# Optimization experiments

Measured on AMD Instinct MI355X. Metric: run time of the kernel, lower is better.

The kernel has to match this reference:

```python
import jax, jax.numpy as jnp
import numpy as np

T, B, F = 160, 640, 40          # time-major input [T, B, F]
H, PJ, L = 768, 256, 3          # nb_hidden, nb_proj, nb_layers
FORGET_BIAS = 1.0               # TF LSTMCell default


def _glorot(k, shape):
    std = (2.0 / (shape[0] + shape[1])) ** 0.5
    return jax.random.normal(k, shape, jnp.float32) * std


def setup_inputs() -> dict:
    key = jax.random.key(0)
    ks = jax.random.split(key, 7)
    x = jax.random.normal(ks[0], (T, B, F), jnp.float32)
    # layer 0: input dim F + proj state PJ; layers 1,2: input dim PJ + PJ
    W0 = _glorot(ks[1], (F + PJ, 4 * H)); b0 = jnp.zeros((4 * H,), jnp.float32)
    P0 = _glorot(ks[2], (H, PJ))
    W1 = _glorot(ks[3], (PJ + PJ, 4 * H)); b1 = jnp.zeros((4 * H,), jnp.float32)
    P1 = _glorot(ks[4], (H, PJ))
    W2 = _glorot(ks[5], (PJ + PJ, 4 * H)); b2 = jnp.zeros((4 * H,), jnp.float32)
    P2 = _glorot(ks[6], (H, PJ))
    return {"x": x, "W0": W0, "b0": b0, "P0": P0,
            "W1": W1, "b1": b1, "P1": P1,
            "W2": W2, "b2": b2, "P2": P2}


def _cell(xt, c, h, W, b, P):
    # TF LSTMCell with num_proj: gates on [x, m_prev]; gate order i, j, f, o.
    z = jnp.concatenate([xt, h], axis=-1) @ W + b            # [B, 4H]
    i, j, f, o = jnp.split(z, 4, axis=-1)
    c_new = jax.nn.sigmoid(f + FORGET_BIAS) * c + jax.nn.sigmoid(i) * jnp.tanh(j)
    m = jax.nn.sigmoid(o) * jnp.tanh(c_new)                  # [B, H]
    h_new = m @ P                                            # projected state [B, PJ]
    return c_new, h_new


def reference(x, W0, b0, P0, W1, b1, P1, W2, b2, P2):
    params = ((W0, b0, P0), (W1, b1, P1), (W2, b2, P2))
    Bd = x.shape[1]
    init = tuple((jnp.zeros((Bd, H), x.dtype), jnp.zeros((Bd, PJ), x.dtype))
                 for _ in range(L))

    def step(carry, xt):
        inp = xt
        new = []
        for (c, h), (W, b, P) in zip(carry, params):
            c, h = _cell(inp, c, h, W, b, P)
            new.append((c, h))
            inp = h
        return tuple(new), None

    carry, _ = jax.lax.scan(step, init, x)
    emb = carry[-1][1]                                       # last layer h at final step, [B, PJ]
    # tf.nn.l2_normalize
    return emb / jnp.sqrt(jnp.maximum(jnp.sum(emb * emb, axis=-1, keepdims=True), 1e-12))
```

## Files before the change

kernel.cpp:

```cpp
#include <hip/hip_runtime.h>

#define Bdim 640
#define Hdim 768
#define PJdim 256
#define Tdim 160
#define NSTEP (Tdim + 2)
#define ZS 258

typedef _Float16 half8 __attribute__((ext_vector_type(8)));
typedef float floatx4 __attribute__((ext_vector_type(4)));

constexpr size_t HB_HALFS = 3ull * Bdim * PJdim;
constexpr size_t ZP_OFF   = HB_HALFS * 2;
constexpr size_t MB_OFF   = ZP_OFF + 256;
constexpr size_t MB_HALFS = 3ull * Bdim * Hdim;
constexpr size_t X_OFF    = MB_OFF + MB_HALFS * 2;
constexpr size_t X_HALFS  = (size_t)Tdim * Bdim * 40;
constexpr size_t W_OFF    = X_OFF + X_HALFS * 2;
constexpr size_t W_HALFS  = 36ull * 131072;
constexpr size_t P_OFF    = W_OFF + W_HALFS * 2;
constexpr size_t P_HALFS  = 3ull * 196608;
constexpr size_t C_OFF    = P_OFF + P_HALFS * 2;
constexpr size_t C_BYTES  = 3ull * Bdim * Hdim * 4;

__device__ __forceinline__ float sigm(float v) { return 1.0f / (1.0f + __expf(-v)); }
__device__ __forceinline__ float tanh_fast(float v) { return 2.0f / (1.0f + __expf(-2.0f * v)) - 1.0f; }

__device__ __forceinline__ uint4 ld_coh16(const void* p) {
    const unsigned long long* q = (const unsigned long long*)p;
    unsigned long long a = __hip_atomic_load(q,     __ATOMIC_RELAXED, __HIP_MEMORY_SCOPE_AGENT);
    unsigned long long b = __hip_atomic_load(q + 1, __ATOMIC_RELAXED, __HIP_MEMORY_SCOPE_AGENT);
    uint4 r; r.x = (unsigned)a; r.y = (unsigned)(a >> 32);
    r.z = (unsigned)b; r.w = (unsigned)(b >> 32);
    return r;
}
__device__ __forceinline__ void st_coh16b(void* p, _Float16 h) {
    union { _Float16 h; unsigned short u; } cv; cv.h = h;
    __hip_atomic_store((unsigned short*)p, cv.u, __ATOMIC_RELAXED, __HIP_MEMORY_SCOPE_AGENT);
}

__device__ __forceinline__ void wait1(unsigned* c, unsigned tgt)
{
    if (threadIdx.x == 0) {
        while (__hip_atomic_load(c, __ATOMIC_RELAXED, __HIP_MEMORY_SCOPE_AGENT) < tgt)
            __builtin_amdgcn_s_sleep(1);
    }
    asm volatile("buffer_inv sc0" ::: "memory");
    __syncthreads();
}

__device__ __forceinline__ void pipe_wait(unsigned* c0, unsigned t0, unsigned* c1, unsigned t1)
{
    if (threadIdx.x == 0) {
        if (t0)
            while (__hip_atomic_load(c0, __ATOMIC_RELAXED, __HIP_MEMORY_SCOPE_AGENT) < t0)
                __builtin_amdgcn_s_sleep(1);
        if (c1 && t1)
            while (__hip_atomic_load(c1, __ATOMIC_RELAXED, __HIP_MEMORY_SCOPE_AGENT) < t1)
                __builtin_amdgcn_s_sleep(1);
    }
    asm volatile("buffer_inv sc0" ::: "memory");
    __syncthreads();
}

__device__ __forceinline__ void pipe_sig(unsigned* c)
{
    __syncthreads();
    if (threadIdx.x == 0)
        __hip_atomic_fetch_add(c, 1u, __ATOMIC_RELAXED, __HIP_MEMORY_SCOPE_AGENT);
}

__global__ void repack_kernel(const float* __restrict__ x,
                              const float* __restrict__ W0, const float* __restrict__ W1,
                              const float* __restrict__ W2, const float* __restrict__ P0,
                              const float* __restrict__ P1, const float* __restrict__ P2,
                              _Float16* __restrict__ Wfrag, _Float16* __restrict__ Pfrag,
                              _Float16* __restrict__ x16)
{
    size_t idx = (size_t)blockIdx.x * 256 + threadIdx.x;
    if (idx < W_HALFS) {
        int slab = (int)(idx >> 17);
        int l = slab / 12, ht = slab % 12;
        int r  = (int)(idx & 131071);
        int kc = r >> 13;
        int r2 = r & 8191;
        int g  = r2 >> 11;
        int cf = (r2 >> 9) & 3;
        int u  = r2 & 511;
        int lane = u >> 3, e = u & 7;
        int qd = lane >> 4, ln = lane & 15;
        int k   = kc * 32 + qd * 8 + e;
        int col = g * Hdim + ht * 64 + cf * 16 + ln;
        float v;
        if (l == 0)      v = (k < 296) ? W0[(size_t)k * 3072 + col] : 0.0f;
        else if (l == 1) v = W1[(size_t)k * 3072 + col];
        else             v = W2[(size_t)k * 3072 + col];
        Wfrag[idx] = (_Float16)v;
    } else if (idx < W_HALFS + P_HALFS) {
        size_t i = idx - W_HALFS;
        int l = (int)(i / 196608);
        int r = (int)(i % 196608);
        int cq = r / 49152;
        int r2 = r % 49152;
        int kc = r2 / 2048;
        int r3 = r2 & 2047;
        int cgr = r3 >> 9;
        int u  = r3 & 511;
        int lane = u >> 3, e = u & 7;
        int qd = lane >> 4, ln = lane & 15;
        int k  = kc * 32 + qd * 8 + e;
        int pj = cq * 64 + cgr * 16 + ln;
        const float* P = (l == 0) ? P0 : (l == 1) ? P1 : P2;
        Pfrag[i] = (_Float16)P[(size_t)k * PJdim + pj];
    } else if (idx < W_HALFS + P_HALFS + X_HALFS) {
        size_t i = idx - W_HALFS - P_HALFS;
        x16[i] = (_Float16)x[i];
    }
}

__device__ __forceinline__ void gate_step(
    int l, int b0r, int h0, int t, bool xl,
    const half8 (&Breg)[16][2], float (&c)[16],
    const _Float16* __restrict__ x16, const _Float16* __restrict__ h16,
    const _Float16* __restrict__ zerop, _Float16* __restrict__ mbuf,
    _Float16* __restrict__ Ast, float* __restrict__ zst, const float* __restrict__ bst,
    unsigned* pd, unsigned pdt, unsigned* pdlo, unsigned pdlot, int tid)
{
    const int wv = tid >> 6, lane = tid & 63, qd = lane >> 4, ln = lane & 15;
    const int g = wv >> 1, hh = wv & 1;
    const int qd8 = qd * 8;
    const int rowg = b0r + wv * 16 + ln;

    const _Float16* xt  = x16 + ((size_t)t * Bdim + rowg) * 40;
    const _Float16* h0b = h16 + (size_t)rowg * PJdim - 40;
    const _Float16* lob = (l > 0) ? h16 + ((size_t)(l - 1) * Bdim + rowg) * PJdim : nullptr;
    const _Float16* hib = h16 + ((size_t)l * Bdim + rowg) * PJdim - 256;

    auto srcp = [&](int kc) -> const _Float16* {
        int k = kc * 32 + qd8;
        if (l == 0) return (k < 40) ? xt + k : (k < 296) ? h0b + k : zerop;
        return (k < 256) ? lob + k : hib + k;
    };

    floatx4 acc[8][2];
    const floatx4 fz = {0.f, 0.f, 0.f, 0.f};
#pragma unroll
    for (int i = 0; i < 8; ++i) { acc[i][0] = fz; acc[i][1] = fz; }

    _Float16* Aw = Ast + wv * 512 + lane * 8;

    auto stage_gemm = [&](int kc0, int nkc, bool coh) {
        const int ncp = nkc >> 1;
        uint4 p0 = coh ? ld_coh16(srcp(kc0))     : *(const uint4*)srcp(kc0);
        uint4 p1 = coh ? ld_coh16(srcp(kc0 + 1)) : *(const uint4*)srcp(kc0 + 1);
#pragma unroll
        for (int cp = 0; cp < 5; ++cp) {
            if (cp < ncp) {
                const int s0 = (cp & 1) * 2;
                *(uint4*)(Aw + (size_t)s0 * 4096)       = p0;
                *(uint4*)(Aw + (size_t)(s0 + 1) * 4096) = p1;
                if (cp + 1 < ncp) {
                    p0 = coh ? ld_coh16(srcp(kc0 + 2 * cp + 2)) : *(const uint4*)srcp(kc0 + 2 * cp + 2);
                    p1 = coh ? ld_coh16(srcp(kc0 + 2 * cp + 3)) : *(const uint4*)srcp(kc0 + 2 * cp + 3);
                }
                __syncthreads();
#pragma unroll
                for (int j = 0; j < 2; ++j) {
                    const _Float16* Ab = Ast + (size_t)(s0 + j) * 4096;
                    const int kc = kc0 + 2 * cp + j;
#pragma unroll
                    for (int rf = 0; rf < 8; ++rf) {
                        half8 af = *(const half8*)(Ab + rf * 512 + lane * 8);
                        acc[rf][0] = __builtin_amdgcn_mfma_f32_16x16x32_f16(af, Breg[kc][0], acc[rf][0], 0, 0, 0);
                        acc[rf][1] = __builtin_amdgcn_mfma_f32_16x16x32_f16(af, Breg[kc][1], acc[rf][1], 0, 0, 0);
                    }
                }
            }
        }
    };

    if (pd) wait1(pd, pdt);
    if (l == 0) {
        stage_gemm(0, 10, false);
    } else {
        stage_gemm(8, 8, false);
        if (pdlo) wait1(pdlo, pdlot);
        stage_gemm(0, 8, xl);
    }
    __syncthreads();

#pragma unroll
    for (int rf = 0; rf < 8; ++rf)
#pragma unroll
        for (int cf = 0; cf < 2; ++cf)
#pragma unroll
            for (int r = 0; r < 4; ++r)
                zst[(size_t)(rf * 16 + qd * 4 + r) * ZS + g * 64 + hh * 32 + cf * 16 + ln]
                    = acc[rf][cf][r];
    __syncthreads();

    const int row = tid >> 2, c0 = (tid & 3) * 16;
    const float* zrow = zst + (size_t)row * ZS;
    union { _Float16 h[16]; uint4 v[2]; } pk;
#pragma unroll
    for (int q = 0; q < 4; ++q) {
        const int o = q * 4;
        float4 zi = *(const float4*)(zrow + c0 + o);
        float4 zj = *(const float4*)(zrow + 64 + c0 + o);
        float4 zf = *(const float4*)(zrow + 128 + c0 + o);
        float4 zo = *(const float4*)(zrow + 192 + c0 + o);
        float4 bi = *(const float4*)(bst + c0 + o);
        float4 bj = *(const float4*)(bst + 64 + c0 + o);
        float4 bf = *(const float4*)(bst + 128 + c0 + o);
        float4 bo = *(const float4*)(bst + 192 + c0 + o);
        float cn0 = sigm(zf.x + bf.x) * c[o + 0] + sigm(zi.x + bi.x) * tanh_fast(zj.x + bj.x);
        float cn1 = sigm(zf.y + bf.y) * c[o + 1] + sigm(zi.y + bi.y) * tanh_fast(zj.y + bj.y);
        float cn2 = sigm(zf.z + bf.z) * c[o + 2] + sigm(zi.z + bi.z) * tanh_fast(zj.z + bj.z);
        float cn3 = sigm(zf.w + bf.w) * c[o + 3] + sigm(zi.w + bi.w) * tanh_fast(zj.w + bj.w);
        c[o + 0] = cn0; c[o + 1] = cn1; c[o + 2] = cn2; c[o + 3] = cn3;
        pk.h[o + 0] = (_Float16)(sigm(zo.x + bo.x) * tanh_fast(cn0));
        pk.h[o + 1] = (_Float16)(sigm(zo.y + bo.y) * tanh_fast(cn1));
        pk.h[o + 2] = (_Float16)(sigm(zo.z + bo.z) * tanh_fast(cn2));
        pk.h[o + 3] = (_Float16)(sigm(zo.w + bo.w) * tanh_fast(cn3));
    }
    _Float16* mb = mbuf + ((size_t)l * Bdim + b0r + row) * Hdim + h0 + c0;
    *(uint4*)mb       = pk.v[0];
    *(uint4*)(mb + 8) = pk.v[1];
}

__device__ __forceinline__ void proj_step(
    int l, int b0r, int cq, const half8 (&Preg)[24],
    const _Float16* __restrict__ mbuf, _Float16* __restrict__ h16,
    _Float16* __restrict__ AstA, _Float16* __restrict__ AstB, int tid, bool xstore)
{
    const int wv = tid >> 6, lane = tid & 63, qd = lane >> 4, ln = lane & 15;
    const int rh = wv >> 2, cgi = wv & 3;
    const int rowg = b0r + wv * 16 + ln;
    const _Float16* mrow = mbuf + ((size_t)l * Bdim + rowg) * Hdim + qd * 8;
    _Float16* wA = AstA + wv * 512 + lane * 8;
    _Float16* wB = AstB + wv * 512 + lane * 8;

    floatx4 pacc[4];
    const floatx4 fz = {0.f, 0.f, 0.f, 0.f};
#pragma unroll
    for (int i = 0; i < 4; ++i) pacc[i] = fz;

    uint4 p0 = *(const uint4*)(mrow);
    uint4 p1 = *(const uint4*)(mrow + 32);
    uint4 p2 = *(const uint4*)(mrow + 64);
    uint4 p3 = *(const uint4*)(mrow + 96);
#pragma unroll
    for (int ch = 0; ch < 6; ++ch) {
        _Float16* W = (ch & 1) ? wB : wA;
        const _Float16* R = (ch & 1) ? AstB : AstA;
        *(uint4*)(W)                      = p0;
        *(uint4*)(W + (size_t)1 * 4096)   = p1;
        *(uint4*)(W + (size_t)2 * 4096)   = p2;
        *(uint4*)(W + (size_t)3 * 4096)   = p3;
        if (ch < 5) {
            p0 = *(const uint4*)(mrow + (4 * ch + 4) * 32);
            p1 = *(const uint4*)(mrow + (4 * ch + 5) * 32);
            p2 = *(const uint4*)(mrow + (4 * ch + 6) * 32);
            p3 = *(const uint4*)(mrow + (4 * ch + 7) * 32);
        }
        __syncthreads();
#pragma unroll
        for (int kk = 0; kk < 4; ++kk) {
            const _Float16* Ab = R + (size_t)kk * 4096;
#pragma unroll
            for (int rfl = 0; rfl < 4; ++rfl) {
                half8 af = *(const half8*)(Ab + (rh * 4 + rfl) * 512 + lane * 8);
                pacc[rfl] = __builtin_amdgcn_mfma_f32_16x16x32_f16(af, Preg[ch * 4 + kk], pacc[rfl], 0, 0, 0);
            }
        }
    }

    if (xstore) {
#pragma unroll
        for (int rfl = 0; rfl < 4; ++rfl)
#pragma unroll
            for (int r = 0; r < 4; ++r) {
                int row = b0r + (rh * 4 + rfl) * 16 + qd * 4 + r;
                st_coh16b(h16 + ((size_t)l * Bdim + row) * PJdim + cq * 64 + cgi * 16 + ln,
                          (_Float16)pacc[rfl][r]);
            }
    } else {
#pragma unroll
        for (int rfl = 0; rfl < 4; ++rfl)
#pragma unroll
            for (int r = 0; r < 4; ++r) {
                int row = b0r + (rh * 4 + rfl) * 16 + qd * 4 + r;
                h16[((size_t)l * Bdim + row) * PJdim + cq * 64 + cgi * 16 + ln] = (_Float16)pacc[rfl][r];
            }
    }
}

__device__ __forceinline__ void load_Breg(const _Float16* __restrict__ Wfrag, int l, int ht,
                                          int wv, int lane, half8 (&Breg)[16][2])
{
    const int g = wv >> 1, hh = wv & 1;
    const _Float16* wslab = Wfrag + ((size_t)(l * 12 + ht)) * 131072;
#pragma unroll
    for (int kc = 0; kc < 16; ++kc)
#pragma unroll
        for (int cf = 0; cf < 2; ++cf)
            Breg[kc][cf] = *(const half8*)(wslab + kc * 8192 + g * 2048 + (hh * 2 + cf) * 512 + lane * 8);
}

__device__ __forceinline__ void load_Preg(const _Float16* __restrict__ Pfrag, int l, int cq,
                                          int wv, int lane, half8 (&Preg)[24])
{
    const int cgi = wv & 3;
    const _Float16* pslab = Pfrag + (size_t)l * 196608 + (size_t)cq * 49152;
#pragma unroll
    for (int kc = 0; kc < 24; ++kc)
        Preg[kc] = *(const half8*)(pslab + kc * 2048 + cgi * 512 + lane * 8);
}

__device__ __forceinline__ void load_bst(const float* __restrict__ bias, int h0, int tid,
                                         float* __restrict__ bst)
{
    if (tid < 256) {
        int gg = tid >> 6, u = tid & 63;
        bst[tid] = bias[gg * Hdim + h0 + u] + ((gg == 2) ? 1.0f : 0.0f);
    }
}

__device__ __forceinline__ void finalize_row(const _Float16* __restrict__ h16,
                                             float* __restrict__ out, int row, int lane)
{
    const _Float16* e = h16 + ((size_t)2 * Bdim + row) * PJdim + lane * 4;
    float v0 = (float)e[0], v1 = (float)e[1], v2 = (float)e[2], v3 = (float)e[3];
    float ss = v0 * v0 + v1 * v1 + v2 * v2 + v3 * v3;
#pragma unroll
    for (int o = 32; o > 0; o >>= 1) ss += __shfl_xor(ss, o, 64);
    float rs = rsqrtf(fmaxf(ss, 1e-12f));
    float4 o4; o4.x = v0 * rs; o4.y = v1 * rs; o4.z = v2 * rs; o4.w = v3 * rs;
    *(float4*)(out + (size_t)row * PJdim + lane * 4) = o4;
}

__global__ __launch_bounds__(512)
void lstm_persist(const _Float16* __restrict__ x16, const _Float16* __restrict__ Wfrag,
                  const _Float16* __restrict__ Pfrag,
                  const float* __restrict__ bias0, const float* __restrict__ bias1,
                  const float* __restrict__ bias2,
                  _Float16* __restrict__ h16, _Float16* __restrict__ mbuf,
                  const _Float16* __restrict__ zerop, float* __restrict__ out,
                  unsigned* __restrict__ flags)
{
    __shared__ __align__(16) char LDSRAW[133120];
    _Float16* Ast  = (_Float16*)LDSRAW;
    float*    zst  = (float*)LDSRAW;
    float*    bst  = (float*)(LDSRAW + 132096);

    const int tid = threadIdx.x, bid = blockIdx.x;
    const int wv = tid >> 6, lane = tid & 63;

    const int xcd = bid & 7, slot = bid >> 3;
    const int gid = xcd * 2 + (slot >> 4);
    const int rr  = slot & 15;
    if (gid >= 15) return;
    const int bt2 = gid / 3, l = gid % 3;
    const int b0r = bt2 * 128;

    unsigned* gd = flags + (size_t)gid * 64;
    unsigned* pd = gd + 32;

    if (rr < 12) {
        const int ht = rr, h0 = ht * 64;
        const bool xl = ((gid & 1) == 0) && (l > 0);
        half8 Breg[16][2];
        load_Breg(Wfrag, l, ht, wv, lane, Breg);
        load_bst((l == 0) ? bias0 : (l == 1) ? bias1 : bias2, h0, tid, bst);
        float c[16];
#pragma unroll
        for (int u = 0; u < 16; ++u) c[u] = 0.f;
        unsigned* pd_lo = (l > 0) ? flags + (size_t)(gid - 1) * 64 + 32 : nullptr;
        for (int t = 0; t < Tdim; ++t) {
            gate_step(l, b0r, h0, t, xl, Breg, c, x16, h16, zerop, mbuf,
                      Ast, zst, bst,
                      pd, 4u * (unsigned)t,
                      pd_lo, (l > 0) ? 4u * (unsigned)(t + 1) : 0u, tid);
            pipe_sig(gd);
        }
        if (l == 2 && rr < 8) {
            wait1(pd, 4u * (unsigned)Tdim);
            int row0 = b0r + rr * 16 + wv * 2;
            finalize_row(h16, out, row0, lane);
            finalize_row(h16, out, row0 + 1, lane);
        }
    } else {
        const int cq = rr - 12;
        const bool xstore = ((gid & 1) == 1) && (gid + 1 < 15) && ((gid + 1) % 3 != 0);
        half8 Preg[24];
        load_Preg(Pfrag, l, cq, wv, lane, Preg);
        unsigned* gd_hi = (l < 2) ? flags + (size_t)(gid + 1) * 64 : nullptr;
        for (int t = 0; t < Tdim; ++t) {
            pipe_wait(gd, 12u * (unsigned)(t + 1), gd_hi, (l < 2) ? 12u * (unsigned)t : 0u);
            proj_step(l, b0r, cq, Preg, mbuf, h16,
                      Ast, (_Float16*)(LDSRAW + 32768), tid, xstore);
            pipe_sig(pd);
        }
    }
}

__global__ __launch_bounds__(512)
void gate_fb(const _Float16* __restrict__ x16, const _Float16* __restrict__ Wfrag,
             const float* __restrict__ bias0, const float* __restrict__ bias1,
             const float* __restrict__ bias2,
             _Float16* __restrict__ h16, _Float16* __restrict__ mbuf,
             const _Float16* __restrict__ zerop, float* __restrict__ cfb, int s)
{
    __shared__ __align__(16) char LDSRAW[133120];
    _Float16* Ast  = (_Float16*)LDSRAW;
    float*    zst  = (float*)LDSRAW;
    float*    bst  = (float*)(LDSRAW + 132096);
    const int tid = threadIdx.x, bid = blockIdx.x;
    const int ht = bid % 12, z = bid / 12, l = z % 3, bt2 = z / 3;
    const int t = s - l;
    if (t < 0 || t >= Tdim) return;
    const int wv = tid >> 6, lane = tid & 63;
    const int b0r = bt2 * 128, h0 = ht * 64;
    half8 Breg[16][2];
    load_Breg(Wfrag, l, ht, wv, lane, Breg);
    load_bst((l == 0) ? bias0 : (l == 1) ? bias1 : bias2, h0, tid, bst);
    __syncthreads();
    const int row = tid >> 2, c0 = (tid & 3) * 16;
    float c[16];
#pragma unroll
    for (int u = 0; u < 16; ++u)
        c[u] = cfb[((size_t)l * Bdim + b0r + row) * Hdim + h0 + c0 + u];
    gate_step(l, b0r, h0, t, false, Breg, c, x16, h16, zerop, mbuf, Ast, zst, bst,
              nullptr, 0u, nullptr, 0u, tid);
#pragma unroll
    for (int u = 0; u < 16; ++u)
        cfb[((size_t)l * Bdim + b0r + row) * Hdim + h0 + c0 + u] = c[u];
}

__global__ __launch_bounds__(512)
void proj_fb(const _Float16* __restrict__ Pfrag, const _Float16* __restrict__ mbuf,
             _Float16* __restrict__ h16, int s)
{
    __shared__ __align__(16) char LDSRAW[65536];
    const int tid = threadIdx.x, bid = blockIdx.x;
    const int cq = bid & 3, z = bid >> 2, l = z % 3, bt2 = z / 3;
    const int tp = s - l;
    if (tp < 0 || tp >= Tdim) return;
    const int wv = tid >> 6, lane = tid & 63;
    half8 Preg[24];
    load_Preg(Pfrag, l, cq, wv, lane, Preg);
    proj_step(l, bt2 * 128, cq, Preg, mbuf, h16,
              (_Float16*)LDSRAW, (_Float16*)(LDSRAW + 32768), tid, false);
}

__global__ __launch_bounds__(512)
void fin_fb(const _Float16* __restrict__ h16, float* __restrict__ out)
{
    int row = blockIdx.x * 8 + (threadIdx.x >> 6);
    finalize_row(h16, out, row, threadIdx.x & 63);
}

extern "C" void kernel_launch(void* const* d_in, const int* in_sizes, int n_in,
                              void* d_out, int out_size, void* d_ws, size_t ws_size,
                              hipStream_t stream)
{
    (void)in_sizes; (void)n_in; (void)out_size; (void)ws_size;
    const float* x  = (const float*)d_in[0];
    const float* W0 = (const float*)d_in[1];
    const float* b0 = (const float*)d_in[2];
    const float* P0 = (const float*)d_in[3];
    const float* W1 = (const float*)d_in[4];
    const float* b1 = (const float*)d_in[5];
    const float* P1 = (const float*)d_in[6];
    const float* W2 = (const float*)d_in[7];
    const float* b2 = (const float*)d_in[8];
    const float* P2 = (const float*)d_in[9];

    char* ws = (char*)d_ws;
    _Float16* h16   = (_Float16*)(ws);
    _Float16* zerop = (_Float16*)(ws + ZP_OFF);
    _Float16* mbuf  = (_Float16*)(ws + MB_OFF);
    _Float16* x16   = (_Float16*)(ws + X_OFF);
    _Float16* Wfrag = (_Float16*)(ws + W_OFF);
    _Float16* Pfrag = (_Float16*)(ws + P_OFF);
    float*    cfb   = (float*)(ws + C_OFF);
    unsigned* flags = (unsigned*)(ws + C_OFF);
    float*    outp  = (float*)d_out;

    hipMemsetAsync(ws, 0, ZP_OFF + 256, stream);
    hipMemsetAsync(cfb, 0, C_BYTES, stream);

    {
        constexpr size_t total = W_HALFS + P_HALFS + X_HALFS;
        int grid = (int)((total + 255) / 256);
        repack_kernel<<<grid, 256, 0, stream>>>(x, W0, W1, W2, P0, P1, P2, Wfrag, Pfrag, x16);
    }

    int occ = 0;
    hipError_t oe = hipOccupancyMaxActiveBlocksPerMultiprocessor(&occ, lstm_persist, 512, 0);
    bool coop = (oe == hipSuccess && occ >= 1);
    if (coop) {
        void* args[] = { (void*)&x16, (void*)&Wfrag, (void*)&Pfrag,
                         (void*)&b0, (void*)&b1, (void*)&b2,
                         (void*)&h16, (void*)&mbuf, (void*)&zerop, (void*)&outp,
                         (void*)&flags };
        hipError_t le = hipLaunchCooperativeKernel((const void*)lstm_persist,
                                                   dim3(256), dim3(512), args, 0, stream);
        if (le != hipSuccess) { (void)hipGetLastError(); coop = false; }
    }
    if (!coop) {
        for (int s = 0; s < NSTEP; ++s) {
            gate_fb<<<180, 512, 0, stream>>>(x16, Wfrag, b0, b1, b2, h16, mbuf, zerop, cfb, s);
            proj_fb<<<60, 512, 0, stream>>>(Pfrag, mbuf, h16, s);
        }
        fin_fb<<<80, 512, 0, stream>>>(h16, outp);
    }
}
```

Measured before the change: 5.138 ms.

## Use per-hidden-tile flags so projection streams chunks as gate blocks finish

```diff
diff --git a/kernel.cpp b/kernel.cpp
--- a/kernel.cpp
+++ b/kernel.cpp
@@ -49,15 +49,13 @@
     __syncthreads();
 }
 
-__device__ __forceinline__ void pipe_wait(unsigned* c0, unsigned t0, unsigned* c1, unsigned t1)
+__device__ __forceinline__ void wait2(unsigned* a, unsigned* b, unsigned tgt)
 {
     if (threadIdx.x == 0) {
-        if (t0)
-            while (__hip_atomic_load(c0, __ATOMIC_RELAXED, __HIP_MEMORY_SCOPE_AGENT) < t0)
-                __builtin_amdgcn_s_sleep(1);
-        if (c1 && t1)
-            while (__hip_atomic_load(c1, __ATOMIC_RELAXED, __HIP_MEMORY_SCOPE_AGENT) < t1)
-                __builtin_amdgcn_s_sleep(1);
+        while (__hip_atomic_load(a, __ATOMIC_RELAXED, __HIP_MEMORY_SCOPE_AGENT) < tgt)
+            __builtin_amdgcn_s_sleep(1);
+        while (__hip_atomic_load(b, __ATOMIC_RELAXED, __HIP_MEMORY_SCOPE_AGENT) < tgt)
+            __builtin_amdgcn_s_sleep(1);
     }
     asm volatile("buffer_inv sc0" ::: "memory");
     __syncthreads();
@@ -68,6 +66,15 @@
     __syncthreads();
     if (threadIdx.x == 0)
         __hip_atomic_fetch_add(c, 1u, __ATOMIC_RELAXED, __HIP_MEMORY_SCOPE_AGENT);
+}
+
+__device__ __forceinline__ void pipe_sig2(unsigned* a, unsigned* b)
+{
+    __syncthreads();
+    if (threadIdx.x == 0) {
+        __hip_atomic_fetch_add(a, 1u, __ATOMIC_RELAXED, __HIP_MEMORY_SCOPE_AGENT);
+        __hip_atomic_fetch_add(b, 1u, __ATOMIC_RELAXED, __HIP_MEMORY_SCOPE_AGENT);
+    }
 }
 
 __global__ void repack_kernel(const float* __restrict__ x,
@@ -231,7 +238,8 @@
 __device__ __forceinline__ void proj_step(
     int l, int b0r, int cq, const half8 (&Preg)[24],
     const _Float16* __restrict__ mbuf, _Float16* __restrict__ h16,
-    _Float16* __restrict__ AstA, _Float16* __restrict__ AstB, int tid, bool xstore)
+    _Float16* __restrict__ AstA, _Float16* __restrict__ AstB, int tid, bool xstore,
+    unsigned* gdhb, unsigned tgt)
 {
     const int wv = tid >> 6, lane = tid & 63, qd = lane >> 4, ln = lane & 15;
     const int rh = wv >> 2, cgi = wv & 3;
@@ -245,6 +253,7 @@
 #pragma unroll
     for (int i = 0; i < 4; ++i) pacc[i] = fz;
 
+    if (gdhb) wait2(gdhb + 0, gdhb + 16, tgt);
     uint4 p0 = *(const uint4*)(mrow);
     uint4 p1 = *(const uint4*)(mrow + 32);
     uint4 p2 = *(const uint4*)(mrow + 64);
@@ -258,6 +267,8 @@
         *(uint4*)(W + (size_t)2 * 4096)   = p2;
         *(uint4*)(W + (size_t)3 * 4096)   = p3;
         if (ch < 5) {
+            if (gdhb) wait2(gdhb + (size_t)(2 * ch + 2) * 16,
+                            gdhb + (size_t)(2 * ch + 3) * 16, tgt);
             p0 = *(const uint4*)(mrow + (4 * ch + 4) * 32);
             p1 = *(const uint4*)(mrow + (4 * ch + 5) * 32);
             p2 = *(const uint4*)(mrow + (4 * ch + 6) * 32);
@@ -363,25 +374,27 @@
     const int bt2 = gid / 3, l = gid % 3;
     const int b0r = bt2 * 128;
 
-    unsigned* gd = flags + (size_t)gid * 64;
-    unsigned* pd = gd + 32;
+    unsigned* gbase = flags + (size_t)gid * 256;
+    unsigned* gd = gbase;
+    unsigned* pd = gbase + 8;
 
     if (rr < 12) {
         const int ht = rr, h0 = ht * 64;
         const bool xl = ((gid & 1) == 0) && (l > 0);
+        unsigned* gdh_self = gbase + 16 + (size_t)ht * 16;
         half8 Breg[16][2];
         load_Breg(Wfrag, l, ht, wv, lane, Breg);
         load_bst((l == 0) ? bias0 : (l == 1) ? bias1 : bias2, h0, tid, bst);
         float c[16];
 #pragma unroll
         for (int u = 0; u < 16; ++u) c[u] = 0.f;
-        unsigned* pd_lo = (l > 0) ? flags + (size_t)(gid - 1) * 64 + 32 : nullptr;
+        unsigned* pd_lo = (l > 0) ? flags + (size_t)(gid - 1) * 256 + 8 : nullptr;
         for (int t = 0; t < Tdim; ++t) {
             gate_step(l, b0r, h0, t, xl, Breg, c, x16, h16, zerop, mbuf,
                       Ast, zst, bst,
                       pd, 4u * (unsigned)t,
                       pd_lo, (l > 0) ? 4u * (unsigned)(t + 1) : 0u, tid);
-            pipe_sig(gd);
+            pipe_sig2(gd, gdh_self);
         }
         if (l == 2 && rr < 8) {
             wait1(pd, 4u * (unsigned)Tdim);
@@ -392,13 +405,15 @@
     } else {
         const int cq = rr - 12;
         const bool xstore = ((gid & 1) == 1) && (gid + 1 < 15) && ((gid + 1) % 3 != 0);
+        unsigned* gdhb = gbase + 16;
         half8 Preg[24];
         load_Preg(Pfrag, l, cq, wv, lane, Preg);
-        unsigned* gd_hi = (l < 2) ? flags + (size_t)(gid + 1) * 64 : nullptr;
+        unsigned* gd_hi = (l < 2) ? flags + (size_t)(gid + 1) * 256 : nullptr;
         for (int t = 0; t < Tdim; ++t) {
-            pipe_wait(gd, 12u * (unsigned)(t + 1), gd_hi, (l < 2) ? 12u * (unsigned)t : 0u);
+            if (gd_hi && t > 0) wait1(gd_hi, 12u * (unsigned)t);
             proj_step(l, b0r, cq, Preg, mbuf, h16,
-                      Ast, (_Float16*)(LDSRAW + 32768), tid, xstore);
+                      Ast, (_Float16*)(LDSRAW + 32768), tid, xstore,
+                      gdhb, (unsigned)(t + 1));
             pipe_sig(pd);
         }
     }
@@ -450,7 +465,8 @@
     half8 Preg[24];
     load_Preg(Pfrag, l, cq, wv, lane, Preg);
     proj_step(l, bt2 * 128, cq, Preg, mbuf, h16,
-              (_Float16*)LDSRAW, (_Float16*)(LDSRAW + 32768), tid, false);
+              (_Float16*)LDSRAW, (_Float16*)(LDSRAW + 32768), tid, false,
+              nullptr, 0u);
 }
 
 __global__ __launch_bounds__(512)
```

Result: no change. 5.143 ms (+0.1%).
